# Kernel tuning notes

Measured on AMD Instinct MI355X. Metric: run time of the kernel, lower is better.

Reference implementation:

```python
import jax, jax.numpy as jnp
import numpy as np

NQ = 4          # n_qubits
NL = 2          # ansatz layers in timestep circuit
T = 200         # n_timesteps
DEG = 3         # qsvt_degree
B = 2048        # batch
NROTS = 5 * NQ * NL     # 40
QFF_NROTS = 5 * NQ      # 20
DIM = 2 ** NQ

# --- batched 2x2 gate matrices (h = theta/2, shape (N,)) ---
def _rx(h):
    c = jnp.cos(h).astype(jnp.complex64)
    s = (-1j * jnp.sin(h)).astype(jnp.complex64)
    return jnp.stack([jnp.stack([c, s], -1), jnp.stack([s, c], -1)], -2)

def _ry(h):
    c, s = jnp.cos(h), jnp.sin(h)
    return jnp.stack([jnp.stack([c, -s], -1), jnp.stack([s, c], -1)], -2).astype(jnp.complex64)

def _rz(h):
    e = jnp.exp(-1j * h.astype(jnp.complex64))
    z = jnp.zeros_like(e)
    return jnp.stack([jnp.stack([e, z], -1), jnp.stack([z, jnp.conj(e)], -1)], -2)

# state layout: (N, 2, 2, ..., 2) with axis 1+w = qubit w (PennyLane wire ordering)
def _apply_1q(state, mat, w):
    st = jnp.moveaxis(state, 1 + w, -1)
    st = jnp.einsum('bij,b...j->b...i', mat, st)
    return jnp.moveaxis(st, -1, 1 + w)

def _apply_crx(state, h, cw, tw):
    m = _rx(h)
    st = jnp.moveaxis(state, (1 + cw, 1 + tw), (-2, -1))  # (..., control, target)
    s1 = jnp.einsum('bij,b...j->b...i', m, st[..., 1, :])  # RX on target iff control=1
    st = jnp.stack([st[..., 0, :], s1], axis=-2)
    return jnp.moveaxis(st, (-2, -1), (1 + cw, 1 + tw))

def _ansatz(state, params, layers):
    # params: (N, 5*NQ*layers) float
    half = params * 0.5
    idx = 0
    for _ in range(layers):
        for i in range(NQ):
            state = _apply_1q(state, _rx(half[:, idx]), i)
            state = _apply_1q(state, _ry(half[:, idx + 1]), i)
            state = _apply_1q(state, _rz(half[:, idx + 2]), i)
            idx += 3
        for i in range(NQ):
            state = _apply_crx(state, half[:, idx], i, (i + 1) % NQ)
            idx += 1
        for i in range(NQ - 1, -1, -1):
            state = _apply_crx(state, half[:, idx], i, (i - 1) % NQ)
            idx += 1
    return state

def _lcu(base, tparams, coeffs):
    # base: (B, DIM) complex; tparams: (B, T, NROTS); coeffs: (B, T) complex
    b, t, r = tparams.shape
    flat = tparams.reshape(b * t, r)
    st = jnp.repeat(base, t, axis=0).reshape((b * t,) + (2,) * NQ)
    st = _ansatz(st, flat, NL)
    ev = st.reshape(b, t, DIM)
    return jnp.einsum('bti,bt->bi', ev, coeffs)

def _expvals(state):
    # returns (B, 3*NQ): [<X_0..X_{n-1}>, <Y...>, <Z...>]
    outs_x, outs_y, outs_z = [], [], []
    red = tuple(range(1, NQ))  # reduce all non-batch, non-target axes after moveaxis
    for i in range(NQ):
        st = jnp.moveaxis(state, 1 + i, -1)
        s0, s1 = st[..., 0], st[..., 1]
        z = jnp.conj(s0) * s1
        outs_x.append(jnp.sum(2.0 * jnp.real(z), axis=red))
        outs_y.append(jnp.sum(2.0 * jnp.imag(z), axis=red))
        outs_z.append(jnp.sum(jnp.abs(s0) ** 2 - jnp.abs(s1) ** 2, axis=red))
    return jnp.stack(outs_x + outs_y + outs_z, axis=1).astype(jnp.float32)

def _forward(timestep_params, poly_coeffs, mix_re, mix_im, qff_params):
    b = timestep_params.shape[0]
    base = jnp.zeros((b, DIM), jnp.complex64).at[:, 0].set(1.0)
    coeffs = jnp.broadcast_to((mix_re + 1j * mix_im).astype(jnp.complex64), (b, T))
    # QSVT polynomial: acc = sum_k c_k (LCU)^k |0>
    acc = poly_coeffs[0] * base
    work = base
    for k in range(1, DEG + 1):
        work = _lcu(work, timestep_params, coeffs)
        acc = acc + poly_coeffs[k] * work
    acc = acc / jnp.sum(jnp.abs(poly_coeffs))  # L1 norm of poly coeffs
    norm = jnp.linalg.norm(acc, axis=1, keepdims=True)
    st = (acc / (norm + 1e-9)).reshape((b,) + (2,) * NQ)
    qp = jnp.broadcast_to(qff_params, (b, QFF_NROTS))
    st = _ansatz(st, qp, 1)
    return _expvals(st)

def setup_inputs() -> dict:
    key = jax.random.key(0)
    k1, k2, k3, k4, k5 = jax.random.split(key, 5)
    return {
        'timestep_params': jax.random.uniform(k1, (B, T, NROTS), jnp.float32),
        'poly_coeffs': jax.random.uniform(k2, (DEG + 1,), jnp.float32),
        'mix_re': jax.random.uniform(k3, (T,), jnp.float32),
        'mix_im': jax.random.uniform(k4, (T,), jnp.float32),
        'qff_params': jax.random.uniform(k5, (QFF_NROTS,), jnp.float32),
    }

def reference(timestep_params, poly_coeffs, mix_re, mix_im, qff_params):
    return _forward(timestep_params, poly_coeffs, mix_re, mix_im, qff_params)
```

## Files before the change

### kernel.cpp

```cpp
#include <hip/hip_runtime.h>
#include <math.h>

#define TSTEPS 200
#define NROTS  40
#define BLK    256
#define DEG    3

__device__ __forceinline__ void fsc(float h, float& s, float& c) {
    s = __sinf(h); c = __cosf(h);
}

__device__ __forceinline__ void make_u(float h1, float h2, float h3, float* u) {
    float s1, c1, s2, c2, s3, c3;
    fsc(h1, s1, c1); fsc(h2, s2, c2); fsc(h3, s3, c3);
    float A = c1 * c2, Bv = s1 * s2, C = c1 * s2, D = s1 * c2;
    u[0] =  c3 * A + s3 * Bv;
    u[1] =  c3 * Bv - s3 * A;
    u[2] = -(c3 * C + s3 * D);
    u[3] =  s3 * C - c3 * D;
}

template<int BIT>
__device__ __forceinline__ void g_u2(float* V, const float* u) {
    const float u00r = u[0], u00i = u[1], u01r = u[2], u01i = u[3];
    #pragma unroll
    for (int p = 0; p < 16; ++p) {
        if (p & BIT) continue;
        const int q = p | BIT;
        float a0r = V[p], a0i = V[16 + p], a1r = V[q], a1i = V[16 + q];
        V[p]      =  u00r * a0r - u00i * a0i + u01r * a1r - u01i * a1i;
        V[16 + p] =  u00r * a0i + u00i * a0r + u01r * a1i + u01i * a1r;
        V[q]      = -u01r * a0r - u01i * a0i + u00r * a1r + u00i * a1i;
        V[16 + q] = -u01r * a0i + u01i * a0r + u00r * a1i - u00i * a1r;
    }
}

template<int CBIT, int TBIT>
__device__ __forceinline__ void g_crx_pre(float* V, float s, float c) {
    #pragma unroll
    for (int p = 0; p < 16; ++p) {
        if (!(p & CBIT) || (p & TBIT)) continue;
        const int q = p | TBIT;
        float a0r = V[p], a0i = V[16 + p], a1r = V[q], a1i = V[16 + q];
        V[p]      = c * a0r + s * a1i;
        V[16 + p] = c * a0i - s * a1r;
        V[q]      = c * a1r + s * a0i;
        V[16 + q] = c * a1i - s * a0r;
    }
}

__device__ __forceinline__ void apply_layer_pre(float* V, const float (&u)[4][4],
                                                const float (&cs)[8][2]) {
    g_u2<8>(V, u[0]); g_u2<4>(V, u[1]); g_u2<2>(V, u[2]); g_u2<1>(V, u[3]);
    g_crx_pre<8, 4>(V, cs[0][0], cs[0][1]);
    g_crx_pre<4, 2>(V, cs[1][0], cs[1][1]);
    g_crx_pre<2, 1>(V, cs[2][0], cs[2][1]);
    g_crx_pre<1, 8>(V, cs[3][0], cs[3][1]);
    g_crx_pre<1, 2>(V, cs[4][0], cs[4][1]);
    g_crx_pre<2, 4>(V, cs[5][0], cs[5][1]);
    g_crx_pre<4, 8>(V, cs[6][0], cs[6][1]);
    g_crx_pre<8, 1>(V, cs[7][0], cs[7][1]);
}

template<int S, int HALF>
__device__ __forceinline__ void rstep(float* V, int lane) {
    const bool hi = (lane >> S) & 1;
    #pragma unroll
    for (int j = 0; j < HALF; ++j) {
        float send = hi ? V[j] : V[j + HALF];
        float keep = hi ? V[j + HALF] : V[j];
        V[j] = keep + __shfl_xor(send, 1 << S, 64);
    }
}

extern "C" __global__ void __launch_bounds__(BLK)
qac_kernel(const float* __restrict__ tp,
           const float* __restrict__ poly,
           const float* __restrict__ mixr,
           const float* __restrict__ mixi,
           const float* __restrict__ qff,
           float* __restrict__ out)
{
    __shared__ float s_red[4][32];
    __shared__ float s_w[32];
    __shared__ float s_acc[32];

    const int b    = blockIdx.x;
    const int tid  = threadIdx.x;
    const int lane = tid & 63;
    const int wv   = tid >> 6;

    if (tid < 32) {
        s_w[tid]   = (tid == 0) ? 1.f : 0.f;
        s_acc[tid] = (tid == 0) ? poly[0] : 0.f;
    }

    float cr_ = 0.f, ci_ = 0.f;
    if (tid < TSTEPS) { cr_ = mixr[tid]; ci_ = mixi[tid]; }
    const int mt = (tid < TSTEPS) ? tid : (TSTEPS - 1);
    const float4* p4 = (const float4*)(tp + (size_t)b * (TSTEPS * NROTS) + mt * NROTS);

    float tu[2][4][4];
    float tc[2][8][2];
    #pragma unroll
    for (int L = 0; L < 2; ++L) {
        float4 f0 = p4[5*L+0], f1 = p4[5*L+1], f2v = p4[5*L+2], f3 = p4[5*L+3], f4 = p4[5*L+4];
        make_u(0.5f*f0.x,  0.5f*f0.y,  0.5f*f0.z,  tu[L][0]);
        make_u(0.5f*f0.w,  0.5f*f1.x,  0.5f*f1.y,  tu[L][1]);
        make_u(0.5f*f1.z,  0.5f*f1.w,  0.5f*f2v.x, tu[L][2]);
        make_u(0.5f*f2v.y, 0.5f*f2v.z, 0.5f*f2v.w, tu[L][3]);
        fsc(0.5f*f3.x, tc[L][0][0], tc[L][0][1]);
        fsc(0.5f*f3.y, tc[L][1][0], tc[L][1][1]);
        fsc(0.5f*f3.z, tc[L][2][0], tc[L][2][1]);
        fsc(0.5f*f3.w, tc[L][3][0], tc[L][3][1]);
        fsc(0.5f*f4.x, tc[L][4][0], tc[L][4][1]);
        fsc(0.5f*f4.y, tc[L][5][0], tc[L][5][1]);
        fsc(0.5f*f4.z, tc[L][6][0], tc[L][6][1]);
        fsc(0.5f*f4.w, tc[L][7][0], tc[L][7][1]);
    }

    const int vidx = ((lane & 1) << 4) | ((lane & 2) << 2) | (lane & 4) |
                     ((lane & 8) >> 2) | ((lane & 16) >> 4);

    __syncthreads();

    #pragma unroll 1
    for (int k = 1; k <= DEG; ++k) {
        float V[32];
        #pragma unroll
        for (int i = 0; i < 32; ++i) V[i] = s_w[i];

        apply_layer_pre(V, tu[0], tc[0]);
        apply_layer_pre(V, tu[1], tc[1]);

        #pragma unroll
        for (int i = 0; i < 16; ++i) {
            float r = V[i], im = V[16 + i];
            V[i]      = r * cr_ - im * ci_;
            V[16 + i] = r * ci_ + im * cr_;
        }

        rstep<0, 16>(V, lane);
        rstep<1, 8>(V, lane);
        rstep<2, 4>(V, lane);
        rstep<3, 2>(V, lane);
        rstep<4, 1>(V, lane);
        float tot = V[0] + __shfl_xor(V[0], 32, 64);
        if (lane < 32) s_red[wv][vidx] = tot;

        __syncthreads();
        if (tid < 32) {
            float r = s_red[0][tid] + s_red[1][tid] + s_red[2][tid] + s_red[3][tid];
            s_w[tid] = r;
            s_acc[tid] += poly[k] * r;
        }
        __syncthreads();
    }

    if (tid < 16) {
        const int l = tid;
        float l1 = fabsf(poly[0]) + fabsf(poly[1]) + fabsf(poly[2]) + fabsf(poly[3]);
        float inv = 1.f / l1;
        float ar = s_acc[l] * inv, ai = s_acc[16 + l] * inv;
        float n2 = ar * ar + ai * ai;
        #pragma unroll
        for (int o = 1; o < 16; o <<= 1) n2 += __shfl_xor(n2, o, 64);
        float sc = 1.f / (sqrtf(n2) + 1e-9f);
        ar *= sc; ai *= sc;

        float s, c, pr, pi, se, ce, t0;
        #pragma unroll
        for (int w = 0; w < 4; ++w) {
            const int BIT = 8 >> w;
            fsc(0.5f * qff[3 * w + 0], s, c);
            pr = __shfl_xor(ar, BIT, 64); pi = __shfl_xor(ai, BIT, 64);
            t0 = c * ar + s * pi; ai = c * ai - s * pr; ar = t0;
            fsc(0.5f * qff[3 * w + 1], s, c);
            pr = __shfl_xor(ar, BIT, 64); pi = __shfl_xor(ai, BIT, 64);
            se = (l & BIT) ? s : -s;
            t0 = c * ar + se * pr; ai = c * ai + se * pi; ar = t0;
            fsc(0.5f * qff[3 * w + 2], s, c);
            se = (l & BIT) ? s : -s;
            t0 = c * ar - se * ai; ai = c * ai + se * ar; ar = t0;
        }
        #define CRXF(CB, TB, hp) { fsc(0.5f * (hp), s, c);                        \
            pr = __shfl_xor(ar, TB, 64); pi = __shfl_xor(ai, TB, 64);             \
            ce = (l & CB) ? c : 1.f; se = (l & CB) ? s : 0.f;                     \
            t0 = ce * ar + se * pi; ai = ce * ai - se * pr; ar = t0; }
        CRXF(8, 4, qff[12]) CRXF(4, 2, qff[13]) CRXF(2, 1, qff[14]) CRXF(1, 8, qff[15])
        CRXF(1, 2, qff[16]) CRXF(2, 4, qff[17]) CRXF(4, 8, qff[18]) CRXF(8, 1, qff[19])
        #undef CRXF

        float* o = out + (size_t)b * 12;
        #pragma unroll
        for (int w = 0; w < 4; ++w) {
            const int BIT = 8 >> w;
            pr = __shfl_xor(ar, BIT, 64); pi = __shfl_xor(ai, BIT, 64);
            float m = (l & BIT) ? 0.f : 1.f;
            float X = m * 2.f * (ar * pr + ai * pi);
            float Y = m * 2.f * (ar * pi - ai * pr);
            float Z = m * (ar * ar + ai * ai - pr * pr - pi * pi);
            #pragma unroll
            for (int of = 1; of < 16; of <<= 1) {
                X += __shfl_xor(X, of, 64);
                Y += __shfl_xor(Y, of, 64);
                Z += __shfl_xor(Z, of, 64);
            }
            if (l == 0) { o[w] = X; o[4 + w] = Y; o[8 + w] = Z; }
        }
    }
}

extern "C" void kernel_launch(void* const* d_in, const int* in_sizes, int n_in,
                              void* d_out, int out_size, void* d_ws, size_t ws_size,
                              hipStream_t stream) {
    const float* tp   = (const float*)d_in[0];
    const float* poly = (const float*)d_in[1];
    const float* mixr = (const float*)d_in[2];
    const float* mixi = (const float*)d_in[3];
    const float* qff  = (const float*)d_in[4];
    float* out = (float*)d_out;
    const int B = in_sizes[0] / (TSTEPS * NROTS);
    qac_kernel<<<dim3(B), dim3(BLK), 0, stream>>>(tp, poly, mixr, mixi, qff, out);
}
```

Measured before the change: 146.4 us.

## Pack two timesteps per thread with float2 vector math and halve block size

Each thread now handles two timesteps (tid and tid+128) using 2-wide float vectors and explicit FMAs, with the block size reduced from 256 to 128. The intent is to let the compiler emit packed FP32 instructions (v_pk_fma_f32) and to halve the threads and the cross-wave reduction work per batch element. In exchange each thread holds about twice as many registers for the state vectors and gate tables, which may cut occupancy. Of the 256 timestep slots, 56 are padding whose contributions are zeroed by the mixing coefficients.

```diff
diff --git a/kernel.cpp b/kernel.cpp
--- a/kernel.cpp
+++ b/kernel.cpp
@@ -3,54 +3,86 @@
 
 #define TSTEPS 200
 #define NROTS  40
-#define BLK    256
+#define BLK    128
 #define DEG    3
+
+typedef float v2 __attribute__((ext_vector_type(2)));
+
+__device__ __forceinline__ v2 mk2(float a, float b) { v2 r; r.x = a; r.y = b; return r; }
+
+#if __has_builtin(__builtin_elementwise_fma)
+#define FMA2(a, b, c) __builtin_elementwise_fma((a), (b), (c))
+#else
+__device__ __forceinline__ v2 FMA2(v2 a, v2 b, v2 c) {
+#pragma clang fp contract(fast)
+    return a * b + c;
+}
+#endif
+
+__device__ __forceinline__ v2 sin2(v2 h) { return mk2(__sinf(h.x), __sinf(h.y)); }
+__device__ __forceinline__ v2 cos2(v2 h) { return mk2(__cosf(h.x), __cosf(h.y)); }
 
 __device__ __forceinline__ void fsc(float h, float& s, float& c) {
     s = __sinf(h); c = __cosf(h);
 }
 
-__device__ __forceinline__ void make_u(float h1, float h2, float h3, float* u) {
-    float s1, c1, s2, c2, s3, c3;
-    fsc(h1, s1, c1); fsc(h2, s2, c2); fsc(h3, s3, c3);
-    float A = c1 * c2, Bv = s1 * s2, C = c1 * s2, D = s1 * c2;
-    u[0] =  c3 * A + s3 * Bv;
-    u[1] =  c3 * Bv - s3 * A;
-    u[2] = -(c3 * C + s3 * D);
-    u[3] =  s3 * C - c3 * D;
-}
+__device__ __forceinline__ void make_u2(v2 h1, v2 h2, v2 h3, v2* u) {
+    v2 s1 = sin2(h1), c1 = cos2(h1);
+    v2 s2 = sin2(h2), c2 = cos2(h2);
+    v2 s3 = sin2(h3), c3 = cos2(h3);
+    v2 A = c1 * c2, Bv = s1 * s2, C = c1 * s2, D = s1 * c2;
+    u[0] = FMA2(s3, Bv, c3 * A);
+    u[1] = FMA2(-s3, A, c3 * Bv);
+    u[2] = -FMA2(s3, D, c3 * C);
+    u[3] = FMA2(-c3, D, s3 * C);
+}
+
+__device__ __forceinline__ void fsc2(v2 h, v2* sc) { sc[0] = sin2(h); sc[1] = cos2(h); }
 
 template<int BIT>
-__device__ __forceinline__ void g_u2(float* V, const float* u) {
-    const float u00r = u[0], u00i = u[1], u01r = u[2], u01i = u[3];
+__device__ __forceinline__ void g_u2(v2* V, const v2* u) {
+    const v2 u00r = u[0], u00i = u[1], u01r = u[2], u01i = u[3];
     #pragma unroll
     for (int p = 0; p < 16; ++p) {
         if (p & BIT) continue;
         const int q = p | BIT;
-        float a0r = V[p], a0i = V[16 + p], a1r = V[q], a1i = V[16 + q];
-        V[p]      =  u00r * a0r - u00i * a0i + u01r * a1r - u01i * a1i;
-        V[16 + p] =  u00r * a0i + u00i * a0r + u01r * a1i + u01i * a1r;
-        V[q]      = -u01r * a0r - u01i * a0i + u00r * a1r + u00i * a1i;
-        V[16 + q] = -u01r * a0i + u01i * a0r + u00r * a1i - u00i * a1r;
+        v2 a0r = V[p], a0i = V[16 + p], a1r = V[q], a1i = V[16 + q];
+        v2 t0 = u00r * a0r;
+        t0 = FMA2(-u00i, a0i, t0);
+        t0 = FMA2( u01r, a1r, t0);
+        t0 = FMA2(-u01i, a1i, t0);
+        v2 t1 = u00r * a0i;
+        t1 = FMA2( u00i, a0r, t1);
+        t1 = FMA2( u01r, a1i, t1);
+        t1 = FMA2( u01i, a1r, t1);
+        v2 t2 = u00r * a1r;
+        t2 = FMA2( u00i, a1i, t2);
+        t2 = FMA2(-u01r, a0r, t2);
+        t2 = FMA2(-u01i, a0i, t2);
+        v2 t3 = u00r * a1i;
+        t3 = FMA2(-u00i, a1r, t3);
+        t3 = FMA2(-u01r, a0i, t3);
+        t3 = FMA2( u01i, a0r, t3);
+        V[p] = t0; V[16 + p] = t1; V[q] = t2; V[16 + q] = t3;
     }
 }
 
 template<int CBIT, int TBIT>
-__device__ __forceinline__ void g_crx_pre(float* V, float s, float c) {
+__device__ __forceinline__ void g_crx_pre(v2* V, v2 s, v2 c) {
     #pragma unroll
     for (int p = 0; p < 16; ++p) {
         if (!(p & CBIT) || (p & TBIT)) continue;
         const int q = p | TBIT;
-        float a0r = V[p], a0i = V[16 + p], a1r = V[q], a1i = V[16 + q];
-        V[p]      = c * a0r + s * a1i;
-        V[16 + p] = c * a0i - s * a1r;
-        V[q]      = c * a1r + s * a0i;
-        V[16 + q] = c * a1i - s * a0r;
-    }
-}
-
-__device__ __forceinline__ void apply_layer_pre(float* V, const float (&u)[4][4],
-                                                const float (&cs)[8][2]) {
+        v2 a0r = V[p], a0i = V[16 + p], a1r = V[q], a1i = V[16 + q];
+        V[p]      = FMA2( s, a1i, c * a0r);
+        V[16 + p] = FMA2(-s, a1r, c * a0i);
+        V[q]      = FMA2( s, a0i, c * a1r);
+        V[16 + q] = FMA2(-s, a0r, c * a1i);
+    }
+}
+
+__device__ __forceinline__ void apply_layer_pre(v2* V, const v2 (&u)[4][4],
+                                                const v2 (&cs)[8][2]) {
     g_u2<8>(V, u[0]); g_u2<4>(V, u[1]); g_u2<2>(V, u[2]); g_u2<1>(V, u[3]);
     g_crx_pre<8, 4>(V, cs[0][0], cs[0][1]);
     g_crx_pre<4, 2>(V, cs[1][0], cs[1][1]);
@@ -73,7 +105,7 @@
     }
 }
 
-extern "C" __global__ void __launch_bounds__(BLK)
+extern "C" __global__ void __launch_bounds__(BLK, 1)
 qac_kernel(const float* __restrict__ tp,
            const float* __restrict__ poly,
            const float* __restrict__ mixr,
@@ -81,7 +113,7 @@
            const float* __restrict__ qff,
            float* __restrict__ out)
 {
-    __shared__ float s_red[4][32];
+    __shared__ float s_red[2][32];
     __shared__ float s_w[32];
     __shared__ float s_acc[32];
 
@@ -95,28 +127,32 @@
         s_acc[tid] = (tid == 0) ? poly[0] : 0.f;
     }
 
-    float cr_ = 0.f, ci_ = 0.f;
-    if (tid < TSTEPS) { cr_ = mixr[tid]; ci_ = mixi[tid]; }
-    const int mt = (tid < TSTEPS) ? tid : (TSTEPS - 1);
-    const float4* p4 = (const float4*)(tp + (size_t)b * (TSTEPS * NROTS) + mt * NROTS);
-
-    float tu[2][4][4];
-    float tc[2][8][2];
+    const bool vB = (tid + BLK) < TSTEPS;
+    const int  tB = vB ? (tid + BLK) : (TSTEPS - 1);
+    v2 cr_ = mk2(mixr[tid], vB ? mixr[tid + BLK] : 0.f);
+    v2 ci_ = mk2(mixi[tid], vB ? mixi[tid + BLK] : 0.f);
+
+    const float4* p4A = (const float4*)(tp + (size_t)b * (TSTEPS * NROTS) + tid * NROTS);
+    const float4* p4B = (const float4*)(tp + (size_t)b * (TSTEPS * NROTS) + tB * NROTS);
+
+    v2 tu[2][4][4];
+    v2 tc[2][8][2];
     #pragma unroll
     for (int L = 0; L < 2; ++L) {
-        float4 f0 = p4[5*L+0], f1 = p4[5*L+1], f2v = p4[5*L+2], f3 = p4[5*L+3], f4 = p4[5*L+4];
-        make_u(0.5f*f0.x,  0.5f*f0.y,  0.5f*f0.z,  tu[L][0]);
-        make_u(0.5f*f0.w,  0.5f*f1.x,  0.5f*f1.y,  tu[L][1]);
-        make_u(0.5f*f1.z,  0.5f*f1.w,  0.5f*f2v.x, tu[L][2]);
-        make_u(0.5f*f2v.y, 0.5f*f2v.z, 0.5f*f2v.w, tu[L][3]);
-        fsc(0.5f*f3.x, tc[L][0][0], tc[L][0][1]);
-        fsc(0.5f*f3.y, tc[L][1][0], tc[L][1][1]);
-        fsc(0.5f*f3.z, tc[L][2][0], tc[L][2][1]);
-        fsc(0.5f*f3.w, tc[L][3][0], tc[L][3][1]);
-        fsc(0.5f*f4.x, tc[L][4][0], tc[L][4][1]);
-        fsc(0.5f*f4.y, tc[L][5][0], tc[L][5][1]);
-        fsc(0.5f*f4.z, tc[L][6][0], tc[L][6][1]);
-        fsc(0.5f*f4.w, tc[L][7][0], tc[L][7][1]);
+        float4 a0 = p4A[5*L+0], a1 = p4A[5*L+1], a2 = p4A[5*L+2], a3 = p4A[5*L+3], a4 = p4A[5*L+4];
+        float4 b0 = p4B[5*L+0], b1 = p4B[5*L+1], b2 = p4B[5*L+2], b3 = p4B[5*L+3], b4 = p4B[5*L+4];
+        make_u2(mk2(0.5f*a0.x, 0.5f*b0.x), mk2(0.5f*a0.y, 0.5f*b0.y), mk2(0.5f*a0.z, 0.5f*b0.z), tu[L][0]);
+        make_u2(mk2(0.5f*a0.w, 0.5f*b0.w), mk2(0.5f*a1.x, 0.5f*b1.x), mk2(0.5f*a1.y, 0.5f*b1.y), tu[L][1]);
+        make_u2(mk2(0.5f*a1.z, 0.5f*b1.z), mk2(0.5f*a1.w, 0.5f*b1.w), mk2(0.5f*a2.x, 0.5f*b2.x), tu[L][2]);
+        make_u2(mk2(0.5f*a2.y, 0.5f*b2.y), mk2(0.5f*a2.z, 0.5f*b2.z), mk2(0.5f*a2.w, 0.5f*b2.w), tu[L][3]);
+        fsc2(mk2(0.5f*a3.x, 0.5f*b3.x), tc[L][0]);
+        fsc2(mk2(0.5f*a3.y, 0.5f*b3.y), tc[L][1]);
+        fsc2(mk2(0.5f*a3.z, 0.5f*b3.z), tc[L][2]);
+        fsc2(mk2(0.5f*a3.w, 0.5f*b3.w), tc[L][3]);
+        fsc2(mk2(0.5f*a4.x, 0.5f*b4.x), tc[L][4]);
+        fsc2(mk2(0.5f*a4.y, 0.5f*b4.y), tc[L][5]);
+        fsc2(mk2(0.5f*a4.z, 0.5f*b4.z), tc[L][6]);
+        fsc2(mk2(0.5f*a4.w, 0.5f*b4.w), tc[L][7]);
     }
 
     const int vidx = ((lane & 1) << 4) | ((lane & 2) << 2) | (lane & 4) |
@@ -126,31 +162,35 @@
 
     #pragma unroll 1
     for (int k = 1; k <= DEG; ++k) {
-        float V[32];
-        #pragma unroll
-        for (int i = 0; i < 32; ++i) V[i] = s_w[i];
+        v2 V[32];
+        #pragma unroll
+        for (int i = 0; i < 32; ++i) { float t = s_w[i]; V[i] = mk2(t, t); }
 
         apply_layer_pre(V, tu[0], tc[0]);
         apply_layer_pre(V, tu[1], tc[1]);
 
         #pragma unroll
         for (int i = 0; i < 16; ++i) {
-            float r = V[i], im = V[16 + i];
-            V[i]      = r * cr_ - im * ci_;
-            V[16 + i] = r * ci_ + im * cr_;
-        }
-
-        rstep<0, 16>(V, lane);
-        rstep<1, 8>(V, lane);
-        rstep<2, 4>(V, lane);
-        rstep<3, 2>(V, lane);
-        rstep<4, 1>(V, lane);
-        float tot = V[0] + __shfl_xor(V[0], 32, 64);
+            v2 r = V[i], im = V[16 + i];
+            V[i]      = FMA2(-im, ci_, r * cr_);
+            V[16 + i] = FMA2( im, cr_, r * ci_);
+        }
+
+        float S[32];
+        #pragma unroll
+        for (int i = 0; i < 32; ++i) S[i] = V[i].x + V[i].y;
+
+        rstep<0, 16>(S, lane);
+        rstep<1, 8>(S, lane);
+        rstep<2, 4>(S, lane);
+        rstep<3, 2>(S, lane);
+        rstep<4, 1>(S, lane);
+        float tot = S[0] + __shfl_xor(S[0], 32, 64);
         if (lane < 32) s_red[wv][vidx] = tot;
 
         __syncthreads();
         if (tid < 32) {
-            float r = s_red[0][tid] + s_red[1][tid] + s_red[2][tid] + s_red[3][tid];
+            float r = s_red[0][tid] + s_red[1][tid];
             s_w[tid] = r;
             s_acc[tid] += poly[k] * r;
         }
```

Measured after the change: 145.6 us. About the same (-0.5%).
